# Kernel tuning notes

Measured on AMD Instinct MI355X. Metric: run time of the kernel, lower is better.

Reference implementation:

```python
import jax, jax.numpy as jnp
import numpy as np

B, H, S, D = 4, 16, 2048, 64
NEG = -1e9


def setup_inputs() -> dict:
    key = jax.random.key(0)
    kq, kk, kv, km = jax.random.split(key, 4)
    query = jax.random.normal(kq, (B, H, S, D), dtype=jnp.float32)
    k_ = jax.random.normal(kk, (B, H, S, D), dtype=jnp.float32)
    v_ = jax.random.normal(kv, (B, H, S, D), dtype=jnp.float32)
    mask = jax.random.randint(km, (B, S, S), 0, 2, dtype=jnp.int32)
    return {"query": query, "key": k_, "value": v_, "mask": mask}


def reference(query, key, value, mask):
    # scores: [B, H, S, S]
    scale = 1.0 / jnp.sqrt(jnp.asarray(query.shape[-1], query.dtype))
    scores = jnp.einsum('bhqd,bhkd->bhqk', query, key) * scale
    # mask [B,S,S] -> [B,1,S,S], broadcast over heads; masked_fill(mask==0, -1e9)
    scores = jnp.where(mask[:, None, :, :] == 0, jnp.asarray(NEG, scores.dtype), scores)
    attn = jax.nn.softmax(scores, axis=-1)
    return jnp.einsum('bhqk,bhkd->bhqd', attn, value)
```

## Files before the change

kernel.cpp:

```cpp
#include <hip/hip_runtime.h>
#include <stdint.h>


#define SQ 2048
#define DD 64

typedef __attribute__((ext_vector_type(8))) short short8;
typedef __attribute__((ext_vector_type(4))) short bshort4;
typedef __attribute__((ext_vector_type(4))) float f32x4;

union U8 { uint32_t u[4]; short8 s; };
union U4 { uint32_t u[2]; bshort4 s; };

__device__ __forceinline__ uint32_t pk_rne(float lo, float hi) {
  uint32_t a = __builtin_bit_cast(uint32_t, lo) + 0x8000u;
  uint32_t b = __builtin_bit_cast(uint32_t, hi) + 0x8000u;
  return __builtin_amdgcn_perm(b, a, 0x07060302u);
}
__device__ __forceinline__ uint32_t pk_tr(float lo, float hi) {
  return __builtin_amdgcn_perm(__builtin_bit_cast(uint32_t, hi),
                               __builtin_bit_cast(uint32_t, lo), 0x07060302u);
}

#if __has_builtin(__builtin_amdgcn_exp2f)
#define EXP2(x) __builtin_amdgcn_exp2f(x)
#else
#define EXP2(x) __exp2f(x)
#endif

__device__ __forceinline__ f32x4 mfma32(short8 a, short8 b, f32x4 c) {
  return __builtin_amdgcn_mfma_f32_16x16x32_bf16(a, b, c, 0, 0, 0);
}
#if __has_builtin(__builtin_amdgcn_mfma_f32_16x16x16bf16_1k)
__device__ __forceinline__ f32x4 mfma16(bshort4 a, bshort4 b, f32x4 c) {
  return __builtin_amdgcn_mfma_f32_16x16x16bf16_1k(a, b, c, 0, 0, 0);
}
#else
__device__ __forceinline__ f32x4 mfma16(bshort4 a, bshort4 b, f32x4 c) {
  asm("v_mfma_f32_16x16x16_bf16 %0, %1, %2, %0" : "+v"(c) : "v"(a), "v"(b));
  return c;
}
#endif

__device__ __forceinline__ void gload_lds16(const short* g, short* l) {
  __builtin_amdgcn_global_load_lds(
      (const __attribute__((address_space(1))) uint32_t*)g,
      (__attribute__((address_space(3))) uint32_t*)l, 16, 0, 0);
}

__global__ __launch_bounds__(256) void pack_mask_kernel(const int* __restrict__ m,
                                                        uint32_t* __restrict__ bits) {
  const int lane = threadIdx.x & 63;
  const int wid = (blockIdx.x * 256 + threadIdx.x) >> 6;
  const int nw = (gridDim.x * 256) >> 6;
  const size_t total = (size_t)4 * SQ * SQ;
  for (size_t base = (size_t)wid * 64; base < total; base += (size_t)nw * 64) {
    int v = m[base + lane];
    unsigned long long b = __ballot(v != 0);
    if (lane == 0) *(unsigned long long*)&bits[base >> 5] = b;
  }
}

__global__ __launch_bounds__(256) void prep_k_kernel(const float* __restrict__ K,
                                                     short* __restrict__ Kt) {
  int tid = blockIdx.x * 256 + threadIdx.x;
  int l = tid & 63, rk = (tid >> 6) & 7, kt = (tid >> 9) & 31, bh = tid >> 14;
  if (bh >= 64) return;
  int key = kt * 64 + (rk >> 1) * 16 + (l & 15);
  int d0 = (rk & 1) * 32 + (l >> 4) * 8;
  const float* src = K + (size_t)bh * (SQ * DD) + (size_t)key * DD + d0;
  float4 a = ((const float4*)src)[0];
  float4 c = ((const float4*)src)[1];
  U8 w;
  w.u[0] = pk_rne(a.x, a.y); w.u[1] = pk_rne(a.z, a.w);
  w.u[2] = pk_rne(c.x, c.y); w.u[3] = pk_rne(c.z, c.w);
  *(short8*)(Kt + (size_t)tid * 8) = w.s;
}

__global__ __launch_bounds__(256) void prep_v_kernel(const float* __restrict__ V,
                                                     short* __restrict__ Vt) {
  int tid = blockIdx.x * 256 + threadIdx.x;
  int r = tid & 63, rv = (tid >> 6) & 15, kt = (tid >> 10) & 31, bh = tid >> 15;
  if (bh >= 64) return;
  int d = (rv & 3) * 16 + (r & 15);
  int k0 = kt * 64 + (rv >> 2) * 16 + (r >> 4) * 4;
  const float* s = V + (size_t)bh * (SQ * DD) + (size_t)k0 * DD + d;
  U4 w;
  w.u[0] = pk_rne(s[0], s[DD]);
  w.u[1] = pk_rne(s[2 * DD], s[3 * DD]);
  *(bshort4*)(Vt + (size_t)tid * 4) = w.s;
}

__global__ __launch_bounds__(256, 4) void attn_fast(
    const float* __restrict__ Qg, const short* __restrict__ Kt,
    const short* __restrict__ Vt, const uint32_t* __restrict__ bits,
    float* __restrict__ Og) {
  __shared__ __align__(16) short sK[2][4096];
  __shared__ __align__(16) short sV[2][4096];
  __shared__ __align__(8) uint32_t sLut[32];

  const int tid = threadIdx.x;
  const int lane = tid & 63;
  const int wv = tid >> 6;
  const int l15 = lane & 15;
  const int quad = lane >> 4;

  const int bid = blockIdx.x;
  const int h = bid & 15;
  const int qt = (bid >> 4) & 15;
  const int b = bid >> 8;

  if (tid < 16) {
    uint32_t m0 = ((tid & 1) ? 0xFFFFu : 0u) | ((tid & 2) ? 0xFFFF0000u : 0u);
    uint32_t m1 = ((tid & 4) ? 0xFFFFu : 0u) | ((tid & 8) ? 0xFFFF0000u : 0u);
    sLut[tid * 2] = m0;
    sLut[tid * 2 + 1] = m1;
  }

  const size_t bh = (size_t)b * 16 + h;
  const float* Qp = Qg + bh * (size_t)(SQ * DD);
  const short* Kh = Kt + bh * (size_t)(SQ * DD);
  const short* Vh = Vt + bh * (size_t)(SQ * DD);
  float* Op = Og + bh * (size_t)(SQ * DD);
  const int q0w = qt * 128 + wv * 32;
  const int brow = b * SQ;

  const float QS = 0.18033688f;
  const float NC = -17.312340f;
  const f32x4 NCv = {NC, NC, NC, NC};

  U4 onesu; onesu.u[0] = 0x3f803f80u; onesu.u[1] = 0x3f803f80u;
  const bshort4 ones = onesu.s;

  short8 qf[2][2];
#pragma unroll
  for (int g = 0; g < 2; ++g)
#pragma unroll
    for (int dc = 0; dc < 2; ++dc) {
      const float* src = Qp + (size_t)(q0w + g * 16 + l15) * DD + dc * 32 + quad * 8;
      float4 a = *(const float4*)src;
      float4 c = *(const float4*)(src + 4);
      U8 t;
      t.u[0] = pk_rne(a.x * QS, a.y * QS);
      t.u[1] = pk_rne(a.z * QS, a.w * QS);
      t.u[2] = pk_rne(c.x * QS, c.y * QS);
      t.u[3] = pk_rne(c.z * QS, c.w * QS);
      qf[g][dc] = t.s;
    }

  f32x4 o[2][4];
  f32x4 osum[2];
#pragma unroll
  for (int g = 0; g < 2; ++g) {
#pragma unroll
    for (int dc = 0; dc < 4; ++dc) o[g][dc] = (f32x4){0.f, 0.f, 0.f, 0.f};
    osum[g] = (f32x4){0.f, 0.f, 0.f, 0.f};
  }

  const int rk0 = wv * 2, rk1 = wv * 2 + 1;
  const short* kg0 = Kh + rk0 * 512 + lane * 8;
  const short* kg1 = Kh + rk1 * 512 + lane * 8;
  const short* vg0 = Vh + rk0 * 512 + lane * 8;
  const short* vg1 = Vh + rk1 * 512 + lane * 8;

  uint2 mwc[2], mwn[2];
#pragma unroll
  for (int g = 0; g < 2; ++g)
    mwc[g] = *(const uint2*)&bits[(size_t)(brow + q0w + g * 16 + l15) * (SQ / 32)];

  gload_lds16(kg0, &sK[0][rk0 * 512]);
  gload_lds16(kg1, &sK[0][rk1 * 512]);
  gload_lds16(vg0, &sV[0][rk0 * 512]);
  gload_lds16(vg1, &sV[0][rk1 * 512]);

  const int sh0 = quad * 4;
  const int sh1 = quad * 4 + 16;

  for (int kt = 0; kt < SQ / 64; ++kt) {
    const int buf = kt & 1;

    __syncthreads();

    if (kt + 1 < SQ / 64) {
      const int off = (kt + 1) * 4096;
      gload_lds16(kg0 + off, &sK[buf ^ 1][rk0 * 512]);
      gload_lds16(kg1 + off, &sK[buf ^ 1][rk1 * 512]);
      gload_lds16(vg0 + off, &sV[buf ^ 1][rk0 * 512]);
      gload_lds16(vg1 + off, &sV[buf ^ 1][rk1 * 512]);
#pragma unroll
      for (int g = 0; g < 2; ++g)
        mwn[g] = *(const uint2*)&bits[(size_t)(brow + q0w + g * 16 + l15) * (SQ / 32) + (kt + 1) * 2];
    }

    const short* kb_base = &sK[buf][lane * 8];
    const short* vb_base = &sV[buf][lane * 4];

#pragma unroll
    for (int kb = 0; kb < 4; ++kb) {
      short8 kfa = *(const short8*)&kb_base[(kb * 2 + 0) * 512];
      short8 kfb = *(const short8*)&kb_base[(kb * 2 + 1) * 512];
      bshort4 vf[4];
#pragma unroll
      for (int dc = 0; dc < 4; ++dc)
        vf[dc] = *(const bshort4*)&vb_base[(kb * 4 + dc) * 256];
      const int sh = (kb & 1) ? sh1 : sh0;

#pragma unroll
      for (int g = 0; g < 2; ++g) {
        uint32_t w = (kb & 2) ? mwc[g].y : mwc[g].x;
        uint32_t t = (w >> sh) & 15u;
        uint2 msk = *(const uint2*)&sLut[t * 2];
        f32x4 st = mfma32(kfa, qf[g][0], NCv);
        st = mfma32(kfb, qf[g][1], st);
        float p0 = EXP2(st[0]);
        float p1 = EXP2(st[1]);
        float p2 = EXP2(st[2]);
        float p3 = EXP2(st[3]);
        U4 pw;
        pw.u[0] = pk_tr(p0, p1) & msk.x;
        pw.u[1] = pk_tr(p2, p3) & msk.y;
#pragma unroll
        for (int dc = 0; dc < 4; ++dc)
          o[g][dc] = mfma16(pw.s, vf[dc], o[g][dc]);
        osum[g] = mfma16(pw.s, ones, osum[g]);
      }
    }

    if (kt + 1 < SQ / 64) {
#pragma unroll
      for (int g = 0; g < 2; ++g) mwc[g] = mwn[g];
    }
  }

#pragma unroll
  for (int g = 0; g < 2; ++g)
#pragma unroll
    for (int r = 0; r < 4; ++r) {
      float inv = 1.0f / osum[g][r];
      float* dst = Op + (size_t)(q0w + g * 16 + quad * 4 + r) * DD + l15;
      dst[0]  = o[g][0][r] * inv;
      dst[16] = o[g][1][r] * inv;
      dst[32] = o[g][2][r] * inv;
      dst[48] = o[g][3][r] * inv;
    }
}

template <bool USE_BITS>
__global__ __launch_bounds__(256, 2) void attn_fb(
    const float* __restrict__ Qg, const float* __restrict__ Kg,
    const float* __restrict__ Vg, const int* __restrict__ Mg,
    const uint32_t* __restrict__ bits, float* __restrict__ Og) {
  __shared__ __align__(16) short sK[2][64 * 72];
  __shared__ __align__(16) short sVT[2][64 * 72];
  const int tid = threadIdx.x;
  const int lane = tid & 63;
  const int wv = tid >> 6;
  const int l15 = lane & 15;
  const int quad = lane >> 4;
  const int bid = blockIdx.x;
  const int h = bid & 15;
  const int qt = (bid >> 4) & 7;
  const int b = bid >> 7;
  const size_t bh = (size_t)b * 16 + h;
  const float* Qp = Qg + bh * (size_t)(SQ * DD);
  const float* Kp = Kg + bh * (size_t)(SQ * DD);
  const float* Vp = Vg + bh * (size_t)(SQ * DD);
  float* Op = Og + bh * (size_t)(SQ * DD);
  const int q0w = qt * 256 + wv * 64;
  const int brow = b * SQ;
  const float QS = 0.18033688f, NC = -17.312340f;
  const float NINF = -__builtin_inff();
  U4 onesu; onesu.u[0] = 0x3f803f80u; onesu.u[1] = 0x3f803f80u;
  const bshort4 ones = onesu.s;
  short8 qf[4][2];
#pragma unroll
  for (int g = 0; g < 4; ++g)
#pragma unroll
    for (int dc = 0; dc < 2; ++dc) {
      const float* src = Qp + (size_t)(q0w + g * 16 + l15) * DD + dc * 32 + quad * 8;
      float4 a = *(const float4*)src;
      float4 c = *(const float4*)(src + 4);
      U8 t;
      t.u[0] = pk_rne(a.x * QS, a.y * QS); t.u[1] = pk_rne(a.z * QS, a.w * QS);
      t.u[2] = pk_rne(c.x * QS, c.y * QS); t.u[3] = pk_rne(c.z * QS, c.w * QS);
      qf[g][dc] = t.s;
    }
  f32x4 o[4][4]; f32x4 osum[4];
#pragma unroll
  for (int g = 0; g < 4; ++g) {
#pragma unroll
    for (int dc = 0; dc < 4; ++dc) o[g][dc] = (f32x4){0.f, 0.f, 0.f, 0.f};
    osum[g] = (f32x4){0.f, 0.f, 0.f, 0.f};
  }
  const int kr = lane, kcb = wv * 16;
  const int vr2 = (lane & 31) * 2, vcb = wv * 16 + (lane >> 5) * 8;
  const float* kbase = Kp + (size_t)kr * DD + kcb;
  const float* vbase = Vp + (size_t)vr2 * DD + vcb;
  float4 kA, kB, kC, kD, vA, vB, vC, vD;
  uint2 mwc[4], mwn[4];
  {
    const float4* kp = (const float4*)kbase;
    kA = kp[0]; kB = kp[1]; kC = kp[2]; kD = kp[3];
    const float* r0 = vbase;
    vA = ((const float4*)r0)[0]; vB = ((const float4*)r0)[1];
    vC = ((const float4*)(r0 + DD))[0]; vD = ((const float4*)(r0 + DD))[1];
    if (USE_BITS) {
#pragma unroll
      for (int g = 0; g < 4; ++g)
        mwc[g] = *(const uint2*)&bits[(size_t)(brow + q0w + g * 16 + l15) * (SQ / 32)];
    }
    U8 w0, w1;
    w0.u[0] = pk_rne(kA.x, kA.y); w0.u[1] = pk_rne(kA.z, kA.w);
    w0.u[2] = pk_rne(kB.x, kB.y); w0.u[3] = pk_rne(kB.z, kB.w);
    w1.u[0] = pk_rne(kC.x, kC.y); w1.u[1] = pk_rne(kC.z, kC.w);
    w1.u[2] = pk_rne(kD.x, kD.y); w1.u[3] = pk_rne(kD.z, kD.w);
    *(short8*)&sK[0][kr * 72 + kcb] = w0.s;
    *(short8*)&sK[0][kr * 72 + kcb + 8] = w1.s;
    float av[8] = {vA.x, vA.y, vA.z, vA.w, vB.x, vB.y, vB.z, vB.w};
    float bv[8] = {vC.x, vC.y, vC.z, vC.w, vD.x, vD.y, vD.z, vD.w};
#pragma unroll
    for (int j = 0; j < 8; ++j)
      *(uint32_t*)&sVT[0][(vcb + j) * 72 + vr2] = pk_rne(av[j], bv[j]);
  }
  for (int kt = 0; kt < SQ / 64; ++kt) {
    const int buf = kt & 1;
    const int k0 = kt * 64;
    __syncthreads();
    if (kt + 1 < SQ / 64) {
      const float4* kp = (const float4*)(kbase + (size_t)(k0 + 64) * DD);
      kA = kp[0]; kB = kp[1]; kC = kp[2]; kD = kp[3];
      const float* r0 = vbase + (size_t)(k0 + 64) * DD;
      vA = ((const float4*)r0)[0]; vB = ((const float4*)r0)[1];
      vC = ((const float4*)(r0 + DD))[0]; vD = ((const float4*)(r0 + DD))[1];
      if (USE_BITS) {
#pragma unroll
        for (int g = 0; g < 4; ++g)
          mwn[g] = *(const uint2*)&bits[(size_t)(brow + q0w + g * 16 + l15) * (SQ / 32) + (kt + 1) * 2];
      }
    }
    const short* sKb = sK[buf];
    const short* sVb = sVT[buf];
#pragma unroll
    for (int kb = 0; kb < 4; ++kb) {
      short8 kfa = *(const short8*)&sKb[(kb * 16 + l15) * 72 + quad * 8];
      short8 kfb = *(const short8*)&sKb[(kb * 16 + l15) * 72 + 32 + quad * 8];
      bshort4 vf[4];
#pragma unroll
      for (int dc = 0; dc < 4; ++dc)
        vf[dc] = *(const bshort4*)&sVb[(dc * 16 + l15) * 72 + kb * 16 + quad * 4];
#pragma unroll
      for (int g = 0; g < 4; ++g) {
        uint32_t t;
        if (USE_BITS) {
          uint32_t w = (kb & 2) ? mwc[g].y : mwc[g].x;
          t = w >> ((kb & 1) * 16 + quad * 4);
        } else {
          const int* mrow = Mg + (size_t)(brow + q0w + g * 16 + l15) * SQ + k0 + kb * 16 + quad * 4;
          t = (mrow[0] != 0) | ((mrow[1] != 0) << 1) | ((mrow[2] != 0) << 2) |
              ((mrow[3] != 0) << 3);
        }
        f32x4 ci;
        ci[0] = (t & 1) ? NC : NINF;
        ci[1] = (t & 2) ? NC : NINF;
        ci[2] = (t & 4) ? NC : NINF;
        ci[3] = (t & 8) ? NC : NINF;
        f32x4 st = mfma32(kfa, qf[g][0], ci);
        st = mfma32(kfb, qf[g][1], st);
        float p0 = EXP2(st[0]), p1 = EXP2(st[1]), p2 = EXP2(st[2]), p3 = EXP2(st[3]);
        U4 pw;
        pw.u[0] = pk_tr(p0, p1);
        pw.u[1] = pk_tr(p2, p3);
#pragma unroll
        for (int dc = 0; dc < 4; ++dc)
          o[g][dc] = mfma16(pw.s, vf[dc], o[g][dc]);
        osum[g] = mfma16(pw.s, ones, osum[g]);
      }
    }
    if (kt + 1 < SQ / 64) {
      short* dK = (short*)sK[buf ^ 1];
      short* dV = (short*)sVT[buf ^ 1];
      U8 w0, w1;
      w0.u[0] = pk_rne(kA.x, kA.y); w0.u[1] = pk_rne(kA.z, kA.w);
      w0.u[2] = pk_rne(kB.x, kB.y); w0.u[3] = pk_rne(kB.z, kB.w);
      w1.u[0] = pk_rne(kC.x, kC.y); w1.u[1] = pk_rne(kC.z, kC.w);
      w1.u[2] = pk_rne(kD.x, kD.y); w1.u[3] = pk_rne(kD.z, kD.w);
      *(short8*)&dK[kr * 72 + kcb] = w0.s;
      *(short8*)&dK[kr * 72 + kcb + 8] = w1.s;
      float av[8] = {vA.x, vA.y, vA.z, vA.w, vB.x, vB.y, vB.z, vB.w};
      float bv[8] = {vC.x, vC.y, vC.z, vC.w, vD.x, vD.y, vD.z, vD.w};
#pragma unroll
      for (int j = 0; j < 8; ++j)
        *(uint32_t*)&dV[(vcb + j) * 72 + vr2] = pk_rne(av[j], bv[j]);
      if (USE_BITS) {
#pragma unroll
        for (int g = 0; g < 4; ++g) mwc[g] = mwn[g];
      }
    }
  }
#pragma unroll
  for (int g = 0; g < 4; ++g)
#pragma unroll
    for (int r = 0; r < 4; ++r) {
      float inv = 1.0f / osum[g][r];
      float* dst = Op + (size_t)(q0w + g * 16 + quad * 4 + r) * DD + l15;
      dst[0]  = o[g][0][r] * inv;
      dst[16] = o[g][1][r] * inv;
      dst[32] = o[g][2][r] * inv;
      dst[48] = o[g][3][r] * inv;
    }
}

extern "C" void kernel_launch(void* const* d_in, const int* in_sizes, int n_in,
                              void* d_out, int out_size, void* d_ws, size_t ws_size,
                              hipStream_t stream) {
  const float* Q = (const float*)d_in[0];
  const float* K = (const float*)d_in[1];
  const float* V = (const float*)d_in[2];
  const int* M = (const int*)d_in[3];
  float* out = (float*)d_out;

  const size_t bits_bytes = (size_t)4 * SQ * SQ / 8;
  const size_t kv_bytes = (size_t)64 * SQ * DD * 2;
  const size_t full_bytes = bits_bytes + 2 * kv_bytes;

  if (ws_size >= full_bytes) {
    uint32_t* bits = (uint32_t*)d_ws;
    short* Kt = (short*)((char*)d_ws + bits_bytes);
    short* Vt = (short*)((char*)d_ws + bits_bytes + kv_bytes);
    pack_mask_kernel<<<2048, 256, 0, stream>>>(M, bits);
    prep_k_kernel<<<4096, 256, 0, stream>>>(K, Kt);
    prep_v_kernel<<<8192, 256, 0, stream>>>(V, Vt);
    attn_fast<<<4 * (SQ / 128) * 16, 256, 0, stream>>>(Q, Kt, Vt, bits, out);
  } else if (ws_size >= bits_bytes) {
    uint32_t* bits = (uint32_t*)d_ws;
    pack_mask_kernel<<<2048, 256, 0, stream>>>(M, bits);
    attn_fb<true><<<4 * (SQ / 256) * 16, 256, 0, stream>>>(Q, K, V, M, bits, out);
  } else {
    attn_fb<false><<<4 * (SQ / 256) * 16, 256, 0, stream>>>(Q, K, V, M, nullptr, out);
  }
}
```

Before: 276.6 us.

## Use K=32 MFMA for PV product with reordered K/V prepacked layouts

Reorders the prepacked K and V layouts so that two 16-key score tiles combine into one 32-wide bf16 operand. The PV and row-sum products can then use the 16x16x32 MFMA instead of twice as many 16x16x16 MFMAs. This halves the PV MFMA instruction count and widens the V LDS reads to 16 bytes. The prep_v kernel now writes 8 elements per thread with half the grid, and the mask bit extraction is remapped to the new key ordering, which risks a layout mismatch if any index is wrong.

```diff
diff --git a/kernel.cpp b/kernel.cpp
--- a/kernel.cpp
+++ b/kernel.cpp
@@ -66,8 +66,10 @@
   int tid = blockIdx.x * 256 + threadIdx.x;
   int l = tid & 63, rk = (tid >> 6) & 7, kt = (tid >> 9) & 31, bh = tid >> 14;
   if (bh >= 64) return;
-  int key = kt * 64 + (rk >> 1) * 16 + (l & 15);
-  int d0 = (rk & 1) * 32 + (l >> 4) * 8;
+  int group = rk >> 2, sub = (rk >> 1) & 1, half = rk & 1;
+  int i = l & 15;
+  int key = kt * 64 + group * 32 + (i >> 2) * 8 + sub * 4 + (i & 3);
+  int d0 = half * 32 + (l >> 4) * 8;
   const float* src = K + (size_t)bh * (SQ * DD) + (size_t)key * DD + d0;
   float4 a = ((const float4*)src)[0];
   float4 c = ((const float4*)src)[1];
@@ -80,15 +82,18 @@
 __global__ __launch_bounds__(256) void prep_v_kernel(const float* __restrict__ V,
                                                      short* __restrict__ Vt) {
   int tid = blockIdx.x * 256 + threadIdx.x;
-  int r = tid & 63, rv = (tid >> 6) & 15, kt = (tid >> 10) & 31, bh = tid >> 15;
+  int l = tid & 63, rv = (tid >> 6) & 7, kt = (tid >> 9) & 31, bh = tid >> 14;
   if (bh >= 64) return;
-  int d = (rv & 3) * 16 + (r & 15);
-  int k0 = kt * 64 + (rv >> 2) * 16 + (r >> 4) * 4;
-  const float* s = V + (size_t)bh * (SQ * DD) + (size_t)k0 * DD + d;
-  U4 w;
+  int group = rv >> 2, dc = rv & 3;
+  int d = dc * 16 + (l & 15);
+  int key0 = kt * 64 + group * 32 + (l >> 4) * 8;
+  const float* s = V + (size_t)bh * (SQ * DD) + (size_t)key0 * DD + d;
+  U8 w;
   w.u[0] = pk_rne(s[0], s[DD]);
   w.u[1] = pk_rne(s[2 * DD], s[3 * DD]);
-  *(bshort4*)(Vt + (size_t)tid * 4) = w.s;
+  w.u[2] = pk_rne(s[4 * DD], s[5 * DD]);
+  w.u[3] = pk_rne(s[6 * DD], s[7 * DD]);
+  *(short8*)(Vt + (size_t)tid * 8) = w.s;
 }
 
 __global__ __launch_bounds__(256, 4) void attn_fast(
@@ -129,8 +134,10 @@
   const float NC = -17.312340f;
   const f32x4 NCv = {NC, NC, NC, NC};
 
-  U4 onesu; onesu.u[0] = 0x3f803f80u; onesu.u[1] = 0x3f803f80u;
-  const bshort4 ones = onesu.s;
+  U8 ones8u;
+  ones8u.u[0] = 0x3f803f80u; ones8u.u[1] = 0x3f803f80u;
+  ones8u.u[2] = 0x3f803f80u; ones8u.u[3] = 0x3f803f80u;
+  const short8 ones8 = ones8u.s;
 
   short8 qf[2][2];
 #pragma unroll
@@ -173,8 +180,8 @@
   gload_lds16(vg0, &sV[0][rk0 * 512]);
   gload_lds16(vg1, &sV[0][rk1 * 512]);
 
-  const int sh0 = quad * 4;
-  const int sh1 = quad * 4 + 16;
+  const int shA = quad * 8;
+  const int shB = quad * 8 + 4;
 
   for (int kt = 0; kt < SQ / 64; ++kt) {
     const int buf = kt & 1;
@@ -193,36 +200,43 @@
     }
 
     const short* kb_base = &sK[buf][lane * 8];
-    const short* vb_base = &sV[buf][lane * 4];
-
-#pragma unroll
-    for (int kb = 0; kb < 4; ++kb) {
-      short8 kfa = *(const short8*)&kb_base[(kb * 2 + 0) * 512];
-      short8 kfb = *(const short8*)&kb_base[(kb * 2 + 1) * 512];
-      bshort4 vf[4];
+    const short* vb_base = &sV[buf][lane * 8];
+
+#pragma unroll
+    for (int grp = 0; grp < 2; ++grp) {
+      short8 kA0 = *(const short8*)&kb_base[(grp * 4 + 0) * 512];
+      short8 kA1 = *(const short8*)&kb_base[(grp * 4 + 1) * 512];
+      short8 kB0 = *(const short8*)&kb_base[(grp * 4 + 2) * 512];
+      short8 kB1 = *(const short8*)&kb_base[(grp * 4 + 3) * 512];
+      short8 vf[4];
 #pragma unroll
       for (int dc = 0; dc < 4; ++dc)
-        vf[dc] = *(const bshort4*)&vb_base[(kb * 4 + dc) * 256];
-      const int sh = (kb & 1) ? sh1 : sh0;
+        vf[dc] = *(const short8*)&vb_base[(grp * 4 + dc) * 512];
 
 #pragma unroll
       for (int g = 0; g < 2; ++g) {
-        uint32_t w = (kb & 2) ? mwc[g].y : mwc[g].x;
-        uint32_t t = (w >> sh) & 15u;
-        uint2 msk = *(const uint2*)&sLut[t * 2];
-        f32x4 st = mfma32(kfa, qf[g][0], NCv);
-        st = mfma32(kfb, qf[g][1], st);
-        float p0 = EXP2(st[0]);
-        float p1 = EXP2(st[1]);
-        float p2 = EXP2(st[2]);
-        float p3 = EXP2(st[3]);
-        U4 pw;
-        pw.u[0] = pk_tr(p0, p1) & msk.x;
-        pw.u[1] = pk_tr(p2, p3) & msk.y;
+        uint32_t w = grp ? mwc[g].y : mwc[g].x;
+        uint32_t tA = (w >> shA) & 15u;
+        uint32_t tB = (w >> shB) & 15u;
+        uint2 mskA = *(const uint2*)&sLut[tA * 2];
+        uint2 mskB = *(const uint2*)&sLut[tB * 2];
+        f32x4 stA = mfma32(kA0, qf[g][0], NCv);
+        stA = mfma32(kA1, qf[g][1], stA);
+        f32x4 stB = mfma32(kB0, qf[g][0], NCv);
+        stB = mfma32(kB1, qf[g][1], stB);
+        float pA0 = EXP2(stA[0]), pA1 = EXP2(stA[1]);
+        float pA2 = EXP2(stA[2]), pA3 = EXP2(stA[3]);
+        float pB0 = EXP2(stB[0]), pB1 = EXP2(stB[1]);
+        float pB2 = EXP2(stB[2]), pB3 = EXP2(stB[3]);
+        U8 pw;
+        pw.u[0] = pk_tr(pA0, pA1) & mskA.x;
+        pw.u[1] = pk_tr(pA2, pA3) & mskA.y;
+        pw.u[2] = pk_tr(pB0, pB1) & mskB.x;
+        pw.u[3] = pk_tr(pB2, pB3) & mskB.y;
 #pragma unroll
         for (int dc = 0; dc < 4; ++dc)
-          o[g][dc] = mfma16(pw.s, vf[dc], o[g][dc]);
-        osum[g] = mfma16(pw.s, ones, osum[g]);
+          o[g][dc] = mfma32(pw.s, vf[dc], o[g][dc]);
+        osum[g] = mfma32(pw.s, ones8, osum[g]);
       }
     }
 
@@ -429,7 +443,7 @@
     short* Vt = (short*)((char*)d_ws + bits_bytes + kv_bytes);
     pack_mask_kernel<<<2048, 256, 0, stream>>>(M, bits);
     prep_k_kernel<<<4096, 256, 0, stream>>>(K, Kt);
-    prep_v_kernel<<<8192, 256, 0, stream>>>(V, Vt);
+    prep_v_kernel<<<4096, 256, 0, stream>>>(V, Vt);
     attn_fast<<<4 * (SQ / 128) * 16, 256, 0, stream>>>(Q, Kt, Vt, bits, out);
   } else if (ws_size >= bits_bytes) {
     uint32_t* bits = (uint32_t*)d_ws;
```

Result: no change. 272.2 us (-1.6%).
